# Kernel tuning notes

Hardware: AMD Instinct MI355X
Metric: run time of the kernel (lower is better)

## Reference

```python
import jax, jax.numpy as jnp
import numpy as np

N_NODES = 100000
N_EDGES = 1600000
D_IN = 128
D_OUT = 128


def setup_inputs() -> dict:
    key = jax.random.key(0)
    k1, k2, k3, k4, k5, k6 = jax.random.split(key, 6)
    x = jax.random.normal(k1, (N_NODES, D_IN), dtype=jnp.float32)
    rows = jax.random.randint(k2, (N_EDGES,), 0, N_NODES, dtype=jnp.int32)
    cols = jax.random.randint(k3, (N_EDGES,), 0, N_NODES, dtype=jnp.int32)
    vals = jax.random.uniform(k4, (N_EDGES,), dtype=jnp.float32)
    # nn.Linear init: U(-1/sqrt(in), 1/sqrt(in))
    bound = 1.0 / np.sqrt(D_IN)
    W = jax.random.uniform(k5, (D_IN, D_OUT), minval=-bound, maxval=bound, dtype=jnp.float32)
    b = jax.random.uniform(k6, (D_OUT,), minval=-bound, maxval=bound, dtype=jnp.float32)
    return {"x": x, "rows": rows, "cols": cols, "vals": vals, "W": W, "b": b}


def reference(x, rows, cols, vals, W, b):
    # support = fc1(x)  -> [N, D_OUT]
    support = x @ W + b
    # output = adj @ support, adj in COO form (rows, cols, vals)
    msg = support[cols] * vals[:, None]          # [E, D_OUT] gather + scale
    out = jax.ops.segment_sum(msg, rows, num_segments=N_NODES)  # scatter-add
    return out
```

## Files before the change

kernel.cpp:

```cpp
#include <hip/hip_runtime.h>

#define D 128
#define SBMAX 64
#define CSTRIDE 400
#define CHN 4096
#define CAP 2560
#define SP 136

typedef short short8 __attribute__((ext_vector_type(8)));
typedef float floatx4 __attribute__((ext_vector_type(4)));

__device__ inline unsigned short f2bf(float f) {
  unsigned u = __float_as_uint(f);
  u += 0x7fffu + ((u >> 16) & 1u);
  return (unsigned short)(u >> 16);
}

__global__ __launch_bounds__(1024) void prep_kernel(
    const float* __restrict__ W, unsigned short* __restrict__ wf,
    const float* __restrict__ x, unsigned int* __restrict__ xh2,
    const int* __restrict__ rows, int* __restrict__ chunk_sb,
    int n_edges, int nchunks, int nsb, int total4) {
  __shared__ int h[SBMAX];
  const int bid = blockIdx.x;
  const int t = threadIdx.x;

  if (bid < 2) {
    int tid = bid * 1024 + t;
    int ks = tid >> 9;
    int rem = tid & 511;
    int nt = rem >> 6;
    int lane = rem & 63;
    int n = nt * 16 + (lane & 15);
    int k0 = ks * 32 + (lane >> 4) * 8;
    unsigned short v[8];
#pragma unroll
    for (int j = 0; j < 8; ++j) v[j] = f2bf(W[(k0 + j) * D + n]);
    uint4 o;
    o.x = (unsigned)v[0] | ((unsigned)v[1] << 16);
    o.y = (unsigned)v[2] | ((unsigned)v[3] << 16);
    o.z = (unsigned)v[4] | ((unsigned)v[5] << 16);
    o.w = (unsigned)v[6] | ((unsigned)v[7] << 16);
    ((uint4*)wf)[tid] = o;
    return;
  }

  if (bid < 2 + nchunks) {
    if (t < SBMAX) h[t] = 0;
    __syncthreads();
    int c = bid - 2;
    int lo = c * CHN;
    int hi = min(lo + CHN, n_edges);
    for (int i = lo + t; i < hi; i += 1024) atomicAdd(&h[rows[i] >> 11], 1);
    __syncthreads();
    if (t < nsb) chunk_sb[t * CSTRIDE + c] = h[t];
    return;
  }

  const float4* x4 = (const float4*)x;
  int base = (bid - 2 - nchunks) * 4096;
#pragma unroll
  for (int k = 0; k < 4; ++k) {
    int i = base + k * 1024 + t;
    if (i < total4) {
      float4 v = x4[i];
      unsigned lo = (unsigned)f2bf(v.x) | ((unsigned)f2bf(v.y) << 16);
      unsigned hi = (unsigned)f2bf(v.z) | ((unsigned)f2bf(v.w) << 16);
      ((uint2*)xh2)[i] = make_uint2(lo, hi);
    }
  }
}

__global__ __launch_bounds__(1024) void p1_kernel(
    const int* __restrict__ rows, const int* __restrict__ cols,
    const float* __restrict__ vals, const int* __restrict__ chunk_sb,
    int* __restrict__ sb_off, int2* __restrict__ tmp1,
    int n_edges, int nchunks, int nsb) {
  __shared__ int ptot[1024];
  __shared__ int ppre[1024];
  __shared__ int sbt[SBMAX];
  __shared__ int sbo[SBMAX + 1];
  __shared__ int base_s[SBMAX];
  __shared__ int h[SBMAX];
  const int c = blockIdx.x;
  const int t = threadIdx.x;

  {
    int s = t >> 4, g = t & 15;
    int tp = 0, pp = 0;
    if (s < nsb) {
      int strip = (nchunks + 15) >> 4;
      int a = g * strip;
      int b2 = min(a + strip, nchunks);
      const int* rowp = chunk_sb + s * CSTRIDE;
      for (int cc = a; cc < b2; ++cc) {
        int v = rowp[cc];
        tp += v;
        pp += (cc < c) ? v : 0;
      }
    }
    ptot[t] = tp;
    ppre[t] = pp;
  }
  __syncthreads();
  if (t < nsb) {
    int tp = 0, pp = 0;
#pragma unroll
    for (int g = 0; g < 16; ++g) { tp += ptot[(t << 4) + g]; pp += ppre[(t << 4) + g]; }
    sbt[t] = tp;
    base_s[t] = pp;
    h[t] = 0;
  }
  __syncthreads();
  if (t == 0) {
    int run = 0;
    for (int s = 0; s < nsb; ++s) { sbo[s] = run; run += sbt[s]; }
    sbo[nsb] = run;
  }
  __syncthreads();
  if (t < nsb) base_s[t] += sbo[t];
  if (c == 0 && t <= nsb) sb_off[t] = sbo[t];
  __syncthreads();

  int lo = c * CHN;
  int hi = min(lo + CHN, n_edges);
  for (int i = lo + t; i < hi; i += 1024) {
    int r = rows[i];
    int s = r >> 11;
    int l = atomicAdd(&h[s], 1);
    tmp1[base_s[s] + l] =
        make_int2(((r & 2047) << 17) | cols[i], __float_as_int(vals[i]));
  }
}

__global__ __launch_bounds__(1024, 8) void gather_gemm_kernel(
    const uint2* __restrict__ xh, const unsigned short* __restrict__ wf,
    const float* __restrict__ bias, const int* __restrict__ sb_off,
    const int2* __restrict__ tmp1, float* __restrict__ out,
    int n_nodes, int nsb) {
  __shared__ __align__(16) char U[67584];
  __shared__ int cnt[128];
  __shared__ int scn[128];
  __shared__ int rs[129];
  __shared__ float rowsum[128];
  __shared__ int fc;
  unsigned short* ys = (unsigned short*)U;
  int2* ebuf = (int2*)U;
  int2* sbuf = (int2*)(U + 34816);
  unsigned short* wfs = (unsigned short*)(U + 34816);
  const int t = threadIdx.x;

  const int xcd = blockIdx.x & 7;
  const int mg = blockIdx.x >> 3;
  const int jj = mg & 15;
  const int sbi = (mg >> 4) * 8 + xcd;
  if (sbi >= nsb) return;
  const int node0 = ((sbi << 4) + jj) << 7;
  if (node0 >= n_nodes) return;

  const uint4* wf4 = (const uint4*)wf;
  uint4 wfr0 = wf4[t];
  uint4 wfr1 = wf4[t + 1024];

  const int lo = sb_off[sbi];
  const int rne = sb_off[sbi + 1] - lo;
  const int slot = t >> 5;
  const int lane = t & 31;

  if (t < 128) cnt[t] = 0;
  if (t == 0) fc = 0;
  __syncthreads();
  for (int i = t; i < rne; i += 1024) {
    int2 p = tmp1[lo + i];
    int lr = ((unsigned)p.x) >> 17;
    if ((lr >> 7) == jj) {
      int pos = atomicAdd(&fc, 1);
      if (pos < CAP) ebuf[pos] = p;
      atomicAdd(&cnt[lr & 127], 1);
    }
  }
  __syncthreads();
  const int ne = fc;

  if (ne <= CAP) {
    if (t < 128) scn[t] = cnt[t];
    __syncthreads();
#pragma unroll
    for (int d = 1; d < 128; d <<= 1) {
      int v = (t < 128 && t >= d) ? scn[t - d] : 0;
      __syncthreads();
      if (t < 128) scn[t] += v;
      __syncthreads();
    }
    if (t < 128) {
      rs[t] = (t == 0) ? 0 : scn[t - 1];
      cnt[t] = 0;
    }
    __syncthreads();
    if (t == 0) rs[128] = scn[127];
    for (int i = t; i < ne; i += 1024) {
      int2 p = ebuf[i];
      int r = (((unsigned)p.x) >> 17) & 127;
      int l = atomicAdd(&cnt[r], 1);
      sbuf[rs[r] + l] = p;
    }
    __syncthreads();
#pragma unroll
    for (int rr = 0; rr < 4; ++rr) {
      int row = slot + (rr << 5);
      int s = rs[row], e = rs[row + 1];
      float4 acc = make_float4(0.f, 0.f, 0.f, 0.f);
      float rsum = 0.f;
      int i = s;
      for (; i + 4 <= e; i += 4) {
        int2 p0 = sbuf[i + 0];
        int2 p1 = sbuf[i + 1];
        int2 p2 = sbuf[i + 2];
        int2 p3 = sbuf[i + 3];
        uint2 s0 = xh[((size_t)(p0.x & 0x1FFFF) << 5) + lane];
        uint2 s1 = xh[((size_t)(p1.x & 0x1FFFF) << 5) + lane];
        uint2 s2 = xh[((size_t)(p2.x & 0x1FFFF) << 5) + lane];
        uint2 s3 = xh[((size_t)(p3.x & 0x1FFFF) << 5) + lane];
        float v0 = __int_as_float(p0.y), v1 = __int_as_float(p1.y);
        float v2 = __int_as_float(p2.y), v3 = __int_as_float(p3.y);
        rsum += v0 + v1 + v2 + v3;
        acc.x += v0 * __uint_as_float(s0.x << 16);
        acc.y += v0 * __uint_as_float(s0.x & 0xffff0000u);
        acc.z += v0 * __uint_as_float(s0.y << 16);
        acc.w += v0 * __uint_as_float(s0.y & 0xffff0000u);
        acc.x += v1 * __uint_as_float(s1.x << 16);
        acc.y += v1 * __uint_as_float(s1.x & 0xffff0000u);
        acc.z += v1 * __uint_as_float(s1.y << 16);
        acc.w += v1 * __uint_as_float(s1.y & 0xffff0000u);
        acc.x += v2 * __uint_as_float(s2.x << 16);
        acc.y += v2 * __uint_as_float(s2.x & 0xffff0000u);
        acc.z += v2 * __uint_as_float(s2.y << 16);
        acc.w += v2 * __uint_as_float(s2.y & 0xffff0000u);
        acc.x += v3 * __uint_as_float(s3.x << 16);
        acc.y += v3 * __uint_as_float(s3.x & 0xffff0000u);
        acc.z += v3 * __uint_as_float(s3.y << 16);
        acc.w += v3 * __uint_as_float(s3.y & 0xffff0000u);
      }
      for (; i < e; ++i) {
        int2 p = sbuf[i];
        float v = __int_as_float(p.y);
        uint2 sv = xh[((size_t)(p.x & 0x1FFFF) << 5) + lane];
        rsum += v;
        acc.x += v * __uint_as_float(sv.x << 16);
        acc.y += v * __uint_as_float(sv.x & 0xffff0000u);
        acc.z += v * __uint_as_float(sv.y << 16);
        acc.w += v * __uint_as_float(sv.y & 0xffff0000u);
      }
      unsigned u0 = (unsigned)f2bf(acc.x) | ((unsigned)f2bf(acc.y) << 16);
      unsigned u1 = (unsigned)f2bf(acc.z) | ((unsigned)f2bf(acc.w) << 16);
      *((uint2*)(ys + row * SP + lane * 4)) = make_uint2(u0, u1);
      if (lane == 0) rowsum[row] = rsum;
    }
  } else {
#pragma unroll
    for (int rr = 0; rr < 4; ++rr) {
      int row = slot + (rr << 5);
      int tgt = (jj << 7) | row;
      float4 acc = make_float4(0.f, 0.f, 0.f, 0.f);
      float rsum = 0.f;
      for (int i = 0; i < rne; ++i) {
        int2 p = tmp1[lo + i];
        if ((int)(((unsigned)p.x) >> 17) != tgt) continue;
        float v = __int_as_float(p.y);
        uint2 sv = xh[((size_t)(p.x & 0x1FFFF) << 5) + lane];
        rsum += v;
        acc.x += v * __uint_as_float(sv.x << 16);
        acc.y += v * __uint_as_float(sv.x & 0xffff0000u);
        acc.z += v * __uint_as_float(sv.y << 16);
        acc.w += v * __uint_as_float(sv.y & 0xffff0000u);
      }
      unsigned u0 = (unsigned)f2bf(acc.x) | ((unsigned)f2bf(acc.y) << 16);
      unsigned u1 = (unsigned)f2bf(acc.z) | ((unsigned)f2bf(acc.w) << 16);
      *((uint2*)(ys + row * SP + lane * 4)) = make_uint2(u0, u1);
      if (lane == 0) rowsum[row] = rsum;
    }
  }
  __syncthreads();

  uint4* wfs4 = (uint4*)wfs;
  wfs4[t] = wfr0;
  wfs4[t + 1024] = wfr1;
  __syncthreads();

  const int l64 = t & 63;
  const int w = t >> 6;
  const int m = l64 & 15, q = l64 >> 4;
  const int rb = (w & 3) * 32;
  const int cb = (w >> 2) * 32;

  floatx4 acc2[2][2];
#pragma unroll
  for (int rt = 0; rt < 2; ++rt)
#pragma unroll
    for (int ct = 0; ct < 2; ++ct) {
      acc2[rt][ct][0] = 0.f; acc2[rt][ct][1] = 0.f;
      acc2[rt][ct][2] = 0.f; acc2[rt][ct][3] = 0.f;
    }

#pragma unroll
  for (int ks = 0; ks < 4; ++ks) {
    short8 af[2], bfr[2];
#pragma unroll
    for (int rt = 0; rt < 2; ++rt)
      af[rt] = *((const short8*)(ys + (rb + rt * 16 + m) * SP + ks * 32 + q * 8));
#pragma unroll
    for (int ct = 0; ct < 2; ++ct) {
      int nt = (cb >> 4) + ct;
      bfr[ct] = *((const short8*)(wfs + ((ks * 8 + nt) * 64 + l64) * 8));
    }
#pragma unroll
    for (int rt = 0; rt < 2; ++rt)
#pragma unroll
      for (int ct = 0; ct < 2; ++ct)
        acc2[rt][ct] = __builtin_amdgcn_mfma_f32_16x16x32_bf16(
            af[rt], bfr[ct], acc2[rt][ct], 0, 0, 0);
  }

  float b0 = bias[cb + m];
  float b1 = bias[cb + 16 + m];
#pragma unroll
  for (int rt = 0; rt < 2; ++rt)
#pragma unroll
    for (int ct = 0; ct < 2; ++ct) {
      float bc = ct ? b1 : b0;
#pragma unroll
      for (int r = 0; r < 4; ++r) {
        int row = rb + rt * 16 + q * 4 + r;
        int col = cb + ct * 16 + m;
        int node = node0 + row;
        if (node < n_nodes)
          out[(size_t)node * D + col] = acc2[rt][ct][r] + rowsum[row] * bc;
      }
    }
}

extern "C" void kernel_launch(void* const* d_in, const int* in_sizes, int n_in,
                              void* d_out, int out_size, void* d_ws, size_t ws_size,
                              hipStream_t stream) {
  const float* x    = (const float*)d_in[0];
  const int*   rows = (const int*)d_in[1];
  const int*   cols = (const int*)d_in[2];
  const float* vals = (const float*)d_in[3];
  const float* W    = (const float*)d_in[4];
  const float* b    = (const float*)d_in[5];
  float* out = (float*)d_out;

  int n_nodes = in_sizes[0] / D;
  int n_edges = in_sizes[1];
  int nb = (n_nodes + 127) >> 7;
  int nsb = (nb + 15) >> 4;
  int nchunks = (n_edges + CHN - 1) / CHN;
  int total_elems = n_nodes * D;
  int total4 = total_elems >> 2;

  char* ws = (char*)d_ws;
  unsigned short* xh = (unsigned short*)(ws);
  int2* tmp1         = (int2*)(ws + 25600000);
  char* mb           = ws + 38400000;
  int* sb_off        = (int*)(mb);
  unsigned short* wf = (unsigned short*)(mb + 512);
  int* chunk_sb      = (int*)out;

  int cblocks = (total4 + 4095) / 4096;
  prep_kernel<<<dim3(2 + nchunks + cblocks), dim3(1024), 0, stream>>>(
      W, wf, x, (unsigned int*)xh, rows, chunk_sb,
      n_edges, nchunks, nsb, total4);

  p1_kernel<<<dim3(nchunks), dim3(1024), 0, stream>>>(
      rows, cols, vals, chunk_sb, sb_off, tmp1, n_edges, nchunks, nsb);

  int ggrid = ((nsb + 7) >> 3) * 8 * 16;
  gather_gemm_kernel<<<dim3(ggrid), dim3(1024), 0, stream>>>(
      (const uint2*)xh, wf, b, sb_off, tmp1, out, n_nodes, nsb);
}
```

Baseline: 236.5 us.

## Add second radix pass to bucket edges per 128-node block before gather

Adds a second partitioning pass (p2_kernel) that uses per-chunk 128-node-bucket histograms to scatter edges from superblock order into exact per-block buckets. The gather kernel then reads only its own bucket instead of scanning the whole superblock's edges 16 times and filtering them. The x-to-bf16 cast moves into its own kernel, and the workspace layout is reorganised. The cost is an extra pass over the edge list and two more launches.

```diff
diff --git a/kernel.cpp b/kernel.cpp
--- a/kernel.cpp
+++ b/kernel.cpp
@@ -1,8 +1,9 @@
 #include <hip/hip_runtime.h>
 
 #define D 128
+#define NB_MAX 1024
 #define SBMAX 64
-#define CSTRIDE 400
+#define CSTRIDE 512
 #define CHN 4096
 #define CAP 2560
 #define SP 136
@@ -18,10 +19,9 @@
 
 __global__ __launch_bounds__(1024) void prep_kernel(
     const float* __restrict__ W, unsigned short* __restrict__ wf,
-    const float* __restrict__ x, unsigned int* __restrict__ xh2,
-    const int* __restrict__ rows, int* __restrict__ chunk_sb,
-    int n_edges, int nchunks, int nsb, int total4) {
-  __shared__ int h[SBMAX];
+    const int* __restrict__ rows, int* __restrict__ chunk_hist,
+    int* __restrict__ chunk_sb, int n_edges, int nb, int nsb) {
+  __shared__ int h[NB_MAX];
   const int bid = blockIdx.x;
   const int t = threadIdx.x;
 
@@ -45,29 +45,19 @@
     return;
   }
 
-  if (bid < 2 + nchunks) {
-    if (t < SBMAX) h[t] = 0;
-    __syncthreads();
-    int c = bid - 2;
-    int lo = c * CHN;
-    int hi = min(lo + CHN, n_edges);
-    for (int i = lo + t; i < hi; i += 1024) atomicAdd(&h[rows[i] >> 11], 1);
-    __syncthreads();
-    if (t < nsb) chunk_sb[t * CSTRIDE + c] = h[t];
-    return;
-  }
-
-  const float4* x4 = (const float4*)x;
-  int base = (bid - 2 - nchunks) * 4096;
-#pragma unroll
-  for (int k = 0; k < 4; ++k) {
-    int i = base + k * 1024 + t;
-    if (i < total4) {
-      float4 v = x4[i];
-      unsigned lo = (unsigned)f2bf(v.x) | ((unsigned)f2bf(v.y) << 16);
-      unsigned hi = (unsigned)f2bf(v.z) | ((unsigned)f2bf(v.w) << 16);
-      ((uint2*)xh2)[i] = make_uint2(lo, hi);
-    }
+  h[t] = 0;
+  __syncthreads();
+  int c = bid - 2;
+  int lo = c * CHN;
+  int hi = min(lo + CHN, n_edges);
+  for (int i = lo + t; i < hi; i += 1024) atomicAdd(&h[rows[i] >> 7], 1);
+  __syncthreads();
+  for (int b = t; b < nb; b += 1024) chunk_hist[b * CSTRIDE + c] = h[b];
+  if (t < nsb) {
+    int s = 0;
+#pragma unroll
+    for (int k = 0; k < 16; ++k) s += h[(t << 4) + k];
+    chunk_sb[t * CSTRIDE + c] = s;
   }
 }
 
@@ -133,56 +123,130 @@
   }
 }
 
+__global__ __launch_bounds__(1024) void p2_kernel(
+    const int* __restrict__ chunk_hist, const int* __restrict__ sb_off,
+    int* __restrict__ bucket_off, const int2* __restrict__ tmp1,
+    int2* __restrict__ tmp2, int nchunks, int nb, int nsb, int n_edges) {
+  __shared__ int ptot[1024];
+  __shared__ int ppre[1024];
+  __shared__ int pmid[1024];
+  __shared__ int loff[17];
+  __shared__ int wbase[16];
+  __shared__ int hh[16];
+  __shared__ int aab[2];
+  const int s = blockIdx.x >> 4;
+  const int j = blockIdx.x & 15;
+  const int t = threadIdx.x;
+  const int c0 = (nchunks * j) >> 4;
+  const int c1 = (nchunks * (j + 1)) >> 4;
+  const int bb = t >> 6, k = t & 63;
+  const int b = (s << 4) + bb;
+
+  int tp = 0, pp = 0, mp = 0;
+  if (b < nb) {
+    int strip = (nchunks + 63) >> 6;
+    int a0 = k * strip;
+    int a1 = min(a0 + strip, nchunks);
+    const int* rowp = chunk_hist + (size_t)b * CSTRIDE;
+    for (int cc = a0; cc < a1; ++cc) {
+      int v = rowp[cc];
+      tp += v;
+      if (cc < c0) pp += v;
+      else if (cc < c1) mp += v;
+    }
+  }
+  ptot[t] = tp; ppre[t] = pp; pmid[t] = mp;
+  __syncthreads();
+#pragma unroll
+  for (int d = 32; d > 0; d >>= 1) {
+    if (k < d) {
+      ptot[t] += ptot[t + d];
+      ppre[t] += ppre[t + d];
+      pmid[t] += pmid[t + d];
+    }
+    __syncthreads();
+  }
+  if (t == 0) {
+    int run = 0, presum = 0, midsum = 0;
+    for (int q = 0; q < 16; ++q) {
+      loff[q] = run;
+      run += ptot[q << 6];
+      presum += ppre[q << 6];
+      midsum += pmid[q << 6];
+    }
+    loff[16] = run;
+    aab[0] = sb_off[s] + presum;
+    aab[1] = sb_off[s] + presum + midsum;
+  }
+  __syncthreads();
+  if (t < 16) {
+    wbase[t] = sb_off[s] + loff[t] + ppre[t << 6];
+    hh[t] = 0;
+    int bprime = (s << 4) + t;
+    if (j == 0 && bprime < nb) bucket_off[bprime] = sb_off[s] + loff[t];
+  }
+  if (j == 0 && s == 0 && t == 0) bucket_off[nb] = n_edges;
+  __syncthreads();
+
+  const int a = aab[0], bend = aab[1];
+  for (int i = a + t; i < bend; i += 1024) {
+    int2 p = tmp1[i];
+    int bi = (((unsigned)p.x) >> 24) & 15;
+    int l = atomicAdd(&hh[bi], 1);
+    tmp2[wbase[bi] + l] = make_int2(p.x & 0x00FFFFFF, p.y);
+  }
+}
+
+__global__ __launch_bounds__(1024) void xcast_kernel(
+    const float* __restrict__ x, unsigned int* __restrict__ xh2, int total4) {
+  const float4* x4 = (const float4*)x;
+  int base = blockIdx.x * 4096;
+#pragma unroll
+  for (int k = 0; k < 4; ++k) {
+    int i = base + k * 1024 + threadIdx.x;
+    if (i < total4) {
+      float4 v = x4[i];
+      unsigned lo = (unsigned)f2bf(v.x) | ((unsigned)f2bf(v.y) << 16);
+      unsigned hi = (unsigned)f2bf(v.z) | ((unsigned)f2bf(v.w) << 16);
+      ((uint2*)xh2)[i] = make_uint2(lo, hi);
+    }
+  }
+}
+
 __global__ __launch_bounds__(1024, 8) void gather_gemm_kernel(
     const uint2* __restrict__ xh, const unsigned short* __restrict__ wf,
-    const float* __restrict__ bias, const int* __restrict__ sb_off,
-    const int2* __restrict__ tmp1, float* __restrict__ out,
-    int n_nodes, int nsb) {
+    const float* __restrict__ bias, const int* __restrict__ bucket_off,
+    const int2* __restrict__ tmp, float* __restrict__ out, int n_nodes) {
   __shared__ __align__(16) char U[67584];
   __shared__ int cnt[128];
   __shared__ int scn[128];
   __shared__ int rs[129];
   __shared__ float rowsum[128];
-  __shared__ int fc;
   unsigned short* ys = (unsigned short*)U;
   int2* ebuf = (int2*)U;
   int2* sbuf = (int2*)(U + 34816);
   unsigned short* wfs = (unsigned short*)(U + 34816);
   const int t = threadIdx.x;
-
-  const int xcd = blockIdx.x & 7;
-  const int mg = blockIdx.x >> 3;
-  const int jj = mg & 15;
-  const int sbi = (mg >> 4) * 8 + xcd;
-  if (sbi >= nsb) return;
-  const int node0 = ((sbi << 4) + jj) << 7;
-  if (node0 >= n_nodes) return;
+  const int b = blockIdx.x;
 
   const uint4* wf4 = (const uint4*)wf;
   uint4 wfr0 = wf4[t];
   uint4 wfr1 = wf4[t + 1024];
 
-  const int lo = sb_off[sbi];
-  const int rne = sb_off[sbi + 1] - lo;
+  const int lo = bucket_off[b];
+  const int ne = bucket_off[b + 1] - lo;
   const int slot = t >> 5;
   const int lane = t & 31;
 
-  if (t < 128) cnt[t] = 0;
-  if (t == 0) fc = 0;
-  __syncthreads();
-  for (int i = t; i < rne; i += 1024) {
-    int2 p = tmp1[lo + i];
-    int lr = ((unsigned)p.x) >> 17;
-    if ((lr >> 7) == jj) {
-      int pos = atomicAdd(&fc, 1);
-      if (pos < CAP) ebuf[pos] = p;
-      atomicAdd(&cnt[lr & 127], 1);
-    }
-  }
-  __syncthreads();
-  const int ne = fc;
-
   if (ne <= CAP) {
+    if (t < 128) cnt[t] = 0;
+    __syncthreads();
+    for (int i = t; i < ne; i += 1024) {
+      int2 p = tmp[lo + i];
+      ebuf[i] = p;
+      atomicAdd(&cnt[((unsigned)p.x) >> 17], 1);
+    }
+    __syncthreads();
     if (t < 128) scn[t] = cnt[t];
     __syncthreads();
 #pragma unroll
@@ -200,7 +264,7 @@
     if (t == 0) rs[128] = scn[127];
     for (int i = t; i < ne; i += 1024) {
       int2 p = ebuf[i];
-      int r = (((unsigned)p.x) >> 17) & 127;
+      int r = ((unsigned)p.x) >> 17;
       int l = atomicAdd(&cnt[r], 1);
       sbuf[rs[r] + l] = p;
     }
@@ -260,12 +324,11 @@
 #pragma unroll
     for (int rr = 0; rr < 4; ++rr) {
       int row = slot + (rr << 5);
-      int tgt = (jj << 7) | row;
       float4 acc = make_float4(0.f, 0.f, 0.f, 0.f);
       float rsum = 0.f;
-      for (int i = 0; i < rne; ++i) {
-        int2 p = tmp1[lo + i];
-        if ((int)(((unsigned)p.x) >> 17) != tgt) continue;
+      for (int i = 0; i < ne; ++i) {
+        int2 p = tmp[lo + i];
+        if ((int)(((unsigned)p.x) >> 17) != row) continue;
         float v = __int_as_float(p.y);
         uint2 sv = xh[((size_t)(p.x & 0x1FFFF) << 5) + lane];
         rsum += v;
@@ -332,7 +395,7 @@
       for (int r = 0; r < 4; ++r) {
         int row = rb + rt * 16 + q * 4 + r;
         int col = cb + ct * 16 + m;
-        int node = node0 + row;
+        int node = (b << 7) + row;
         if (node < n_nodes)
           out[(size_t)node * D + col] = acc2[rt][ct][r] + rowsum[row] * bc;
       }
@@ -355,26 +418,31 @@
   int nb = (n_nodes + 127) >> 7;
   int nsb = (nb + 15) >> 4;
   int nchunks = (n_edges + CHN - 1) / CHN;
-  int total_elems = n_nodes * D;
-  int total4 = total_elems >> 2;
+  int total4 = (n_nodes * D) >> 2;
 
   char* ws = (char*)d_ws;
-  unsigned short* xh = (unsigned short*)(ws);
+  int2* tmp2         = (int2*)(ws);
+  unsigned short* xh = (unsigned short*)(ws + 12800000);
   int2* tmp1         = (int2*)(ws + 25600000);
   char* mb           = ws + 38400000;
   int* sb_off        = (int*)(mb);
-  unsigned short* wf = (unsigned short*)(mb + 512);
-  int* chunk_sb      = (int*)out;
-
-  int cblocks = (total4 + 4095) / 4096;
-  prep_kernel<<<dim3(2 + nchunks + cblocks), dim3(1024), 0, stream>>>(
-      W, wf, x, (unsigned int*)xh, rows, chunk_sb,
-      n_edges, nchunks, nsb, total4);
+  int* bucket_off    = (int*)(mb + 512);
+  unsigned short* wf = (unsigned short*)(mb + 4608);
+  int* chunk_hist    = (int*)out;
+  int* chunk_sb      = (int*)((char*)out + 1605632);
+
+  prep_kernel<<<dim3(2 + nchunks), dim3(1024), 0, stream>>>(
+      W, wf, rows, chunk_hist, chunk_sb, n_edges, nb, nsb);
 
   p1_kernel<<<dim3(nchunks), dim3(1024), 0, stream>>>(
       rows, cols, vals, chunk_sb, sb_off, tmp1, n_edges, nchunks, nsb);
 
-  int ggrid = ((nsb + 7) >> 3) * 8 * 16;
-  gather_gemm_kernel<<<dim3(ggrid), dim3(1024), 0, stream>>>(
-      (const uint2*)xh, wf, b, sb_off, tmp1, out, n_nodes, nsb);
-}
+  p2_kernel<<<dim3(nsb * 16), dim3(1024), 0, stream>>>(
+      chunk_hist, sb_off, bucket_off, tmp1, tmp2, nchunks, nb, nsb, n_edges);
+
+  xcast_kernel<<<dim3((total4 + 4095) / 4096), dim3(1024), 0, stream>>>(
+      x, (unsigned int*)xh, total4);
+
+  gather_gemm_kernel<<<dim3(nb), dim3(1024), 0, stream>>>(
+      (const uint2*)xh, wf, b, bucket_off, tmp2, out, n_nodes);
+}
```

Result: no change. 232.1 us (-1.9%).
